# Kernel optimization log

Hardware: AMD Instinct MI355X
Metric: run time of the kernel (lower is better)

Reference implementation:

```python
import jax, jax.numpy as jnp
import numpy as np

N_CIR, N_DIS, D, H = 585, 88, 128, 8
E_CC, E_DD = 20000, 3000
EPS = 1e-16


def _gcn(x, src, dst, ew, W, b, N):
    # PyG GCNConv: add self-loops (weight 1), symmetric normalization, x @ W, scatter-add, + bias
    loop = jnp.arange(N)
    s = jnp.concatenate([src, loop])
    d = jnp.concatenate([dst, loop])
    w = jnp.concatenate([ew, jnp.ones((N,), ew.dtype)])
    deg = jax.ops.segment_sum(w, d, num_segments=N)
    dinv = jnp.where(deg > 0, jax.lax.rsqrt(deg), 0.0)
    norm = dinv[s] * w * dinv[d]                      # [E+N]
    h = x @ W                                         # [N,D]
    out = jax.ops.segment_sum(h[s] * norm[:, None], d, num_segments=N)
    return out + b


def _gat(x, src, dst, ea, W, a_src, a_dst, a_edge, We, b, N):
    # PyG GATConv(heads=H, concat=False, edge_dim=1): self-loops with mean edge_attr fill,
    # leaky_relu attention logits, segment softmax over destination, mean over heads, + bias
    loop = jnp.arange(N)
    s = jnp.concatenate([src, loop])
    d = jnp.concatenate([dst, loop])
    ea = jnp.concatenate([ea, jnp.broadcast_to(ea.mean(0, keepdims=True), (N, ea.shape[1]))], 0)
    h = (x @ W).reshape(N, H, D)                      # [N,H,D]
    e = (ea @ We).reshape(-1, H, D)                   # [E+N,H,D]
    alpha = (h * a_src).sum(-1)[s] + (h * a_dst).sum(-1)[d] + (e * a_edge).sum(-1)
    alpha = jax.nn.leaky_relu(alpha, 0.2)             # [E+N,H]
    amax = jax.ops.segment_max(alpha, d, num_segments=N)
    ex = jnp.exp(alpha - amax[d])
    den = jax.ops.segment_sum(ex, d, num_segments=N)
    alpha = ex / (den[d] + EPS)
    out = jax.ops.segment_sum(h[s] * alpha[:, :, None], d, num_segments=N)  # [N,H,D]
    return out.mean(1) + b


def _branch(x, edges, mat, gw1, gb1, aw, asrc, adst, aedge, awe, ab, gw2, gb2, N):
    src, dst = edges[0], edges[1]
    ew = mat[src, dst]                                # gather edge weights from dense matrix
    f1 = jax.nn.relu(_gcn(x, src, dst, ew, gw1, gb1, N))
    att = jax.nn.relu(_gat(f1, src, dst, ew[:, None], aw, asrc, adst, aedge, awe, ab, N))
    f2 = jax.nn.relu(_gcn(att, src, dst, ew, gw2, gb2, N))
    return f1, f2


def _cnn(f1, f2, Wk, b):
    # Conv2d(2,256,(128,1)) over [1,2,128,N] == per-node GEMM over (2,128) then view/transpose
    Xv = jnp.stack([f1.T, f2.T])                      # [2,D,N]
    return jnp.einsum('ock,ckn->no', Wk[..., 0], Xv) + b  # [N,256]


def setup_inputs():
    ks = jax.random.split(jax.random.key(0), 24)
    rn = lambda i, sh, s=1.0: jax.random.normal(ks[i], sh, jnp.float32) * s
    w = 0.08  # ~glorot scale for fan-in 128
    return {
        'x_cir': rn(0, (N_CIR, D)),
        'x_dis': rn(1, (N_DIS, D)),
        'cc_matrix': jax.random.uniform(ks[2], (N_CIR, N_CIR), jnp.float32),
        'dd_matrix': jax.random.uniform(ks[3], (N_DIS, N_DIS), jnp.float32),
        'gcn_c1_w': rn(4, (D, D), w), 'gcn_c1_b': jnp.zeros((D,), jnp.float32),
        'gat_c_w': rn(5, (D, H * D), w), 'gat_c_asrc': rn(6, (H, D), w),
        'gat_c_adst': rn(7, (H, D), w), 'gat_c_aedge': rn(8, (H, D), w),
        'gat_c_we': rn(9, (1, H * D), w), 'gat_c_b': jnp.zeros((D,), jnp.float32),
        'gcn_c2_w': rn(10, (D, D), w), 'gcn_c2_b': jnp.zeros((D,), jnp.float32),
        'gcn_d1_w': rn(11, (D, D), w), 'gcn_d1_b': jnp.zeros((D,), jnp.float32),
        'gat_d_w': rn(12, (D, H * D), w), 'gat_d_asrc': rn(13, (H, D), w),
        'gat_d_adst': rn(14, (H, D), w), 'gat_d_aedge': rn(15, (H, D), w),
        'gat_d_we': rn(16, (1, H * D), w), 'gat_d_b': jnp.zeros((D,), jnp.float32),
        'gcn_d2_w': rn(17, (D, D), w), 'gcn_d2_b': jnp.zeros((D,), jnp.float32),
        'conv_c_w': rn(18, (256, 2, D, 1), w), 'conv_c_b': jnp.zeros((256,), jnp.float32),
        'conv_d_w': rn(19, (256, 2, D, 1), w), 'conv_d_b': jnp.zeros((256,), jnp.float32),
        'cc_edges': jax.random.randint(ks[20], (2, E_CC), 0, N_CIR),
        'dd_edges': jax.random.randint(ks[21], (2, E_DD), 0, N_DIS),
    }


def reference(x_cir, x_dis, cc_matrix, dd_matrix,
              gcn_c1_w, gcn_c1_b, gat_c_w, gat_c_asrc, gat_c_adst, gat_c_aedge, gat_c_we, gat_c_b,
              gcn_c2_w, gcn_c2_b,
              gcn_d1_w, gcn_d1_b, gat_d_w, gat_d_asrc, gat_d_adst, gat_d_aedge, gat_d_we, gat_d_b,
              gcn_d2_w, gcn_d2_b,
              conv_c_w, conv_c_b, conv_d_w, conv_d_b,
              cc_edges, dd_edges):
    c1, c2 = _branch(x_cir, cc_edges, cc_matrix, gcn_c1_w, gcn_c1_b, gat_c_w, gat_c_asrc,
                     gat_c_adst, gat_c_aedge, gat_c_we, gat_c_b, gcn_c2_w, gcn_c2_b, N_CIR)
    d1, d2 = _branch(x_dis, dd_edges, dd_matrix, gcn_d1_w, gcn_d1_b, gat_d_w, gat_d_asrc,
                     gat_d_adst, gat_d_aedge, gat_d_we, gat_d_b, gcn_d2_w, gcn_d2_b, N_DIS)
    cir_fea = _cnn(c1, c2, conv_c_w, conv_c_b)        # [585,256]
    dis_fea = _cnn(d1, d2, conv_d_w, conv_d_b)        # [88,256]
    return cir_fea @ dis_fea.T, cir_fea, dis_fea
```

## Files before the change

### kernel.cpp

```cpp
#include <hip/hip_runtime.h>

constexpr int NCIR = 585;
constexpr int NDIS = 88;
constexpr int NT   = NCIR + NDIS;
constexpr int DIM  = 128;
constexpr int NH   = 8;
constexpr int ECC  = 20000;
constexpr int EDD  = 3000;
constexpr int ET   = ECC + EDD;
constexpr int CO   = 256;
constexpr int CAP  = 256;
constexpr int F1C  = (NCIR + 3) / 4;
constexpr int F1D  = (NDIS + 3) / 4;
constexpr int NG   = F1C + F1D;
constexpr int GBK  = (ET + 255) / 256;
constexpr int GEMB = (NT + 1) / 2;

__device__ __forceinline__ int decode_cnt(unsigned raw){
  return (int)(raw >= 0xA0000000u ? raw - 0xAAAAAAAAu : raw);
}

struct P {
  const float *x_c, *x_d, *mat_c, *mat_d;
  const float *g1w_c, *g1b_c, *aw_c, *as_c, *ad_c, *ae_c, *we_c, *ab_c, *g2w_c, *g2b_c;
  const float *g1w_d, *g1b_d, *aw_d, *as_d, *ad_d, *ae_d, *we_d, *ab_d, *g2w_d, *g2b_d;
  const float *cw_c, *cb_c, *cw_d, *cb_d;
  const int *csrc, *cdst, *dsrc, *ddst;
  float *hs, *hd, *h, *f1, *hg, *fill_w, *psc, *psd, *wdeg;
  unsigned *cnt;
  int *fill_s;
  float *out_score, *out_cir, *out_dis;
};

__global__ __launch_bounds__(256) void k_gg(P p){
  __shared__ float r0[256], r1[256];
  int b = blockIdx.x, t = threadIdx.x;
  if (b < GBK){
    int e = b * 256 + t;
    float wc = 0.0f, wdv = 0.0f;
    if (e < ET){
      float w; int s, d;
      if (e < ECC){
        s = p.csrc[e]; d = p.cdst[e];
        w = p.mat_c[s * NCIR + d]; wc = w;
      } else {
        int el = e - ECC;
        s = NCIR + p.dsrc[el]; d = NCIR + p.ddst[el];
        w = p.mat_d[(s - NCIR) * NDIS + (d - NCIR)]; wdv = w;
      }
      int pos = decode_cnt(atomicAdd(&p.cnt[d], 1u));
      if (pos < CAP){
        p.fill_s[d * CAP + pos] = s;
        p.fill_w[d * CAP + pos] = w;
      }
      atomicAdd(&p.wdeg[d], w);
    }
    r0[t] = wc; r1[t] = wdv;
    __syncthreads();
    for (int st = 128; st; st >>= 1){
      if (t < st){ r0[t] += r0[t + st]; r1[t] += r1[t + st]; }
      __syncthreads();
    }
    if (t == 0){ p.psc[b] = r0[0]; p.psd[b] = r1[0]; }
  } else {
    int ub = (b - GBK) * 2;
    int n = t >> 7, k = t & 127;
    int u = ub + n;
    bool ok = u < NT;
    if (ok){
      int br = u >= NCIR;
      r0[n * DIM + k] = br ? p.x_d[(u - NCIR) * DIM + k] : p.x_c[u * DIM + k];
    }
    __syncthreads();
    if (ok){
      const float* W = (u >= NCIR) ? p.g1w_d : p.g1w_c;
      float acc = 0.0f;
      #pragma unroll 8
      for (int c = 0; c < DIM; ++c) acc += r0[n * DIM + c] * W[c * DIM + k];
      p.h[u * DIM + k] = acc;
    }
  }
}

__global__ __launch_bounds__(256) void k_aggproj(P p){
  __shared__ int   deg4[4];
  __shared__ float dv4[4];
  __shared__ int   s4[4][CAP];
  __shared__ float nrm4[4][CAP];
  __shared__ float a_sh[4][DIM];
  __shared__ float wred[4][8];
  int b = blockIdx.x, t = threadIdx.x;
  int ng = b >> 2, ct = b & 3;
  int base, count, br;
  if (ng < F1C){ base = ng * 4; count = min(4, NCIR - base); br = 0; }
  else { base = NCIR + (ng - F1C) * 4; count = 4; br = 1; }
  if (t < 4){
    if (t < count){
      int u = base + t;
      deg4[t] = min(decode_cnt(p.cnt[u]), CAP);
      dv4[t]  = rsqrtf(1.0f + p.wdeg[u]);
    } else deg4[t] = 0;
  }
  __syncthreads();
  for (int idx = t; idx < 4 * CAP; idx += 256){
    int nn = idx >> 8, j = idx & (CAP - 1);
    if (j < deg4[nn]){
      int u = base + nn;
      int s = p.fill_s[u * CAP + j];
      s4[nn][j] = s;
      nrm4[nn][j] = rsqrtf(1.0f + p.wdeg[s]) * p.fill_w[u * CAP + j] * dv4[nn];
    }
  }
  __syncthreads();
  const float* B1 = br ? p.g1b_d : p.g1b_c;
  int n2 = t >> 7, k = t & 127;
  for (int r = 0; r < 2; ++r){
    int nn = n2 + r * 2;
    float v = 0.0f;
    if (nn < count){
      int u = base + nn;
      float dvu = dv4[nn];
      float acc = B1[k] + p.h[u * DIM + k] * dvu * dvu;
      int deg = deg4[nn];
      #pragma unroll 4
      for (int j = 0; j < deg; ++j)
        acc += p.h[s4[nn][j] * DIM + k] * nrm4[nn][j];
      if (ct == 0) p.f1[u * DIM + k] = acc;
      v = fmaxf(acc, 0.0f);
    }
    a_sh[nn][k] = v;
  }
  __syncthreads();
  const float* W = (br ? p.aw_d : p.aw_c) + ct * 256 + t;
  float acc[4] = {0.f, 0.f, 0.f, 0.f};
  #pragma unroll 4
  for (int c = 0; c < DIM; ++c){
    float w = W[c * 1024];
    acc[0] += a_sh[0][c] * w; acc[1] += a_sh[1][c] * w;
    acc[2] += a_sh[2][c] * w; acc[3] += a_sh[3][c] * w;
  }
  int col = ct * 256 + t;
  for (int n = 0; n < count; ++n)
    p.hg[(size_t)(base + n) * 1024 + col] = acc[n];
  const float* As = br ? p.as_d : p.as_c;
  const float* Ad = br ? p.ad_d : p.ad_c;
  float av = As[col], dw = Ad[col];
  int w = t >> 6;
  #pragma unroll
  for (int n = 0; n < 4; ++n){
    float sdot = acc[n] * av, ddot = acc[n] * dw;
    #pragma unroll
    for (int off = 32; off; off >>= 1){
      sdot += __shfl_down(sdot, off, 64);
      ddot += __shfl_down(ddot, off, 64);
    }
    if ((t & 63) == 0){ wred[w][n * 2] = sdot; wred[w][n * 2 + 1] = ddot; }
  }
  __syncthreads();
  if (t < 16){
    int g = t >> 3, v = t & 7, n = v >> 1, isd = v & 1;
    if (n < count){
      float sum = wred[g * 2][v] + wred[g * 2 + 1][v];
      float* dst = isd ? p.hd : p.hs;
      dst[(base + n) * NH + ct * 2 + g] = sum;
    }
  }
}

__global__ __launch_bounds__(256) void k_att(P p){
  __shared__ float den_sh[NH], hd_sh[NH], inv_sh[NH], wself_sh[NH], wd_sh[NH];
  __shared__ float slw_sh;
  __shared__ int   s_all[CAP];
  __shared__ float w_all[CAP];
  __shared__ float alpha_all[CAP * NH];
  __shared__ float a2[2][DIM], attv[DIM], part[2][DIM];
  int d = blockIdx.x, t = threadIdx.x;
  int g = t >> 7, k = t & 127;
  int br = d >= NCIR;
  int wv = t >> 6, lane = t & 63;
  if (t < NH){ den_sh[t] = 0.0f; hd_sh[t] = p.hd[d * NH + t]; }
  if (wv == 0){
    const float* ps = br ? p.psd : p.psc;
    float v = (lane < GBK ? ps[lane] : 0.0f) + (lane + 64 < GBK ? ps[lane + 64] : 0.0f);
    #pragma unroll
    for (int off = 32; off; off >>= 1) v += __shfl_down(v, off, 64);
    if (lane == 0) slw_sh = v / (br ? (float)EDD : (float)ECC);
  }
  if (wv >= 2){
    const float* We = br ? p.we_d : p.we_c;
    const float* Ae = br ? p.ae_d : p.ae_c;
    for (int q = 0; q < 4; ++q){
      int hh = (wv - 2) * 4 + q;
      float v = We[hh * DIM + lane] * Ae[hh * DIM + lane]
              + We[hh * DIM + 64 + lane] * Ae[hh * DIM + 64 + lane];
      #pragma unroll
      for (int off = 32; off; off >>= 1) v += __shfl_down(v, off, 64);
      if (lane == 0) wd_sh[hh] = v;
    }
  }
  int deg = min(decode_cnt(p.cnt[d]), CAP);
  for (int j = t; j < deg; j += 256){
    s_all[j] = p.fill_s[d * CAP + j];
    w_all[j] = p.fill_w[d * CAP + j];
  }
  __syncthreads();
  for (int idx = t; idx < deg * NH; idx += 256){
    int j = idx >> 3, hh = idx & 7;
    int s = s_all[j];
    float a = p.hs[s * NH + hh] + hd_sh[hh] + w_all[j] * wd_sh[hh];
    a = a > 0.0f ? a : 0.2f * a;
    float ex = expf(a);
    alpha_all[idx] = ex;
    atomicAdd(&den_sh[hh], ex);
  }
  __syncthreads();
  if (t < NH){
    float a = p.hs[d * NH + t] + hd_sh[t] + slw_sh * wd_sh[t];
    a = a > 0.0f ? a : 0.2f * a;
    float ex = expf(a);
    float inv = 1.0f / (den_sh[t] + ex + 1e-16f) * 0.125f;
    inv_sh[t] = inv;
    wself_sh[t] = ex * inv;
  }
  __syncthreads();
  for (int idx = t; idx < deg * NH; idx += 256)
    alpha_all[idx] *= inv_sh[idx & 7];
  __syncthreads();
  float acc = 0.0f;
  if (g == 0){
    acc = (br ? p.ab_d : p.ab_c)[k];
    const float* r = p.hg + (size_t)d * 1024;
    #pragma unroll
    for (int hh = 0; hh < NH; ++hh) acc += wself_sh[hh] * r[hh * DIM + k];
  }
  for (int jj = g; jj < deg; jj += 2){
    const float* r = p.hg + (size_t)s_all[jj] * 1024;
    const float* al = alpha_all + jj * NH;
    #pragma unroll
    for (int hh = 0; hh < NH; ++hh) acc += al[hh] * r[hh * DIM + k];
  }
  a2[g][k] = acc;
  __syncthreads();
  if (g == 0) attv[k] = fmaxf(a2[0][k] + a2[1][k], 0.0f);
  __syncthreads();
  const float* W = br ? p.g2w_d : p.g2w_c;
  float h2 = 0.0f;
  #pragma unroll 8
  for (int c = g * 64; c < g * 64 + 64; ++c) h2 += attv[c] * W[c * DIM + k];
  part[g][k] = h2;
  __syncthreads();
  if (g == 0) p.h[d * DIM + k] = part[0][k] + part[1][k];
}

__global__ __launch_bounds__(256) void k_fuse2(P p){
  __shared__ float s12[4][2 * DIM];
  __shared__ int   deg4[4];
  __shared__ float dv4[4];
  __shared__ int   s4[4][CAP];
  __shared__ float nrm4[4][CAP];
  int b = blockIdx.x, o = threadIdx.x;
  int gbase, count, br; float* out;
  if (b < F1C){ gbase = b * 4; count = min(4, NCIR - gbase); br = 0;
                out = p.out_cir + (size_t)gbase * CO; }
  else { int lb = (b - F1C) * 4; gbase = NCIR + lb; count = 4; br = 1;
         out = p.out_dis + (size_t)lb * CO; }
  if (o < 4){
    if (o < count){
      int u = gbase + o;
      deg4[o] = min(decode_cnt(p.cnt[u]), CAP);
      dv4[o]  = rsqrtf(1.0f + p.wdeg[u]);
    } else deg4[o] = 0;
  }
  __syncthreads();
  for (int idx = o; idx < 4 * CAP; idx += 256){
    int nn = idx >> 8, j = idx & (CAP - 1);
    if (j < deg4[nn]){
      int u = gbase + nn;
      int s = p.fill_s[u * CAP + j];
      s4[nn][j] = s;
      nrm4[nn][j] = rsqrtf(1.0f + p.wdeg[s]) * p.fill_w[u * CAP + j] * dv4[nn];
    }
  }
  __syncthreads();
  const float* B2 = br ? p.g2b_d : p.g2b_c;
  int n2 = o >> 7, k = o & 127;
  for (int r = 0; r < 2; ++r){
    int nn = n2 + r * 2;
    float v1 = 0.0f, v2 = 0.0f;
    if (nn < count){
      int u = gbase + nn;
      float dvu = dv4[nn];
      float acc = B2[k] + p.h[u * DIM + k] * dvu * dvu;
      int deg = deg4[nn];
      #pragma unroll 4
      for (int j = 0; j < deg; ++j)
        acc += p.h[s4[nn][j] * DIM + k] * nrm4[nn][j];
      v2 = fmaxf(acc, 0.0f);
      v1 = fmaxf(p.f1[u * DIM + k], 0.0f);
    }
    s12[nn][k] = v1;
    s12[nn][DIM + k] = v2;
  }
  __syncthreads();
  const float* W = (br ? p.cw_d : p.cw_c) + o * 2 * DIM;
  float bv = (br ? p.cb_d : p.cb_c)[o];
  float a0 = bv, a1 = bv, a2 = bv, a3 = bv;
  #pragma unroll 4
  for (int q = 0; q < 2 * DIM; ++q){
    float wv = W[q];
    a0 += s12[0][q] * wv; a1 += s12[1][q] * wv;
    a2 += s12[2][q] * wv; a3 += s12[3][q] * wv;
  }
  if (0 < count) out[0 * CO + o] = a0;
  if (1 < count) out[1 * CO + o] = a1;
  if (2 < count) out[2 * CO + o] = a2;
  if (3 < count) out[3 * CO + o] = a3;
}

__global__ void k_final(P p){
  __shared__ float ci[CO];
  int i = blockIdx.x, j = threadIdx.x;
  ci[j]       = p.out_cir[i * CO + j];
  ci[DIM + j] = p.out_cir[i * CO + DIM + j];
  __syncthreads();
  if (j < NDIS){
    const float* dr = p.out_dis + j * CO;
    float acc = 0.0f;
    #pragma unroll 8
    for (int q = 0; q < CO; ++q) acc += ci[q] * dr[q];
    p.out_score[i * NDIS + j] = acc;
  }
}

extern "C" void kernel_launch(void* const* d_in, const int* in_sizes, int n_in,
                              void* d_out, int out_size, void* d_ws, size_t ws_size,
                              hipStream_t stream){
  P p;
  typedef const float* F;
  p.x_c   = (F)d_in[0];  p.x_d   = (F)d_in[1];
  p.mat_c = (F)d_in[2];  p.mat_d = (F)d_in[3];
  p.g1w_c = (F)d_in[4];  p.g1b_c = (F)d_in[5];
  p.aw_c  = (F)d_in[6];  p.as_c  = (F)d_in[7];  p.ad_c = (F)d_in[8];
  p.ae_c  = (F)d_in[9];  p.we_c  = (F)d_in[10]; p.ab_c = (F)d_in[11];
  p.g2w_c = (F)d_in[12]; p.g2b_c = (F)d_in[13];
  p.g1w_d = (F)d_in[14]; p.g1b_d = (F)d_in[15];
  p.aw_d  = (F)d_in[16]; p.as_d  = (F)d_in[17]; p.ad_d = (F)d_in[18];
  p.ae_d  = (F)d_in[19]; p.we_d  = (F)d_in[20]; p.ab_d = (F)d_in[21];
  p.g2w_d = (F)d_in[22]; p.g2b_d = (F)d_in[23];
  p.cw_c  = (F)d_in[24]; p.cb_c  = (F)d_in[25];
  p.cw_d  = (F)d_in[26]; p.cb_d  = (F)d_in[27];
  const int* cc_edges = (const int*)d_in[28];
  const int* dd_edges = (const int*)d_in[29];
  p.csrc = cc_edges;  p.cdst = cc_edges + ECC;
  p.dsrc = dd_edges;  p.ddst = dd_edges + EDD;

  float* out = (float*)d_out;
  p.out_score = out;
  p.out_cir   = out + NCIR * NDIS;
  p.out_dis   = p.out_cir + NCIR * CO;

  float* w = (float*)d_ws;
  auto alloc = [&](size_t n){ float* q = w; w += n; return q; };
  p.wdeg   = alloc(676);
  p.cnt    = (unsigned*)alloc(676);
  p.psc    = alloc(92);
  p.psd    = alloc(92);
  p.hs     = alloc((size_t)NT * NH);
  p.hd     = alloc((size_t)NT * NH);
  p.h      = alloc((size_t)NT * DIM);
  p.f1     = alloc((size_t)NT * DIM);
  p.hg     = alloc((size_t)NT * 1024);
  p.fill_w = alloc((size_t)NT * CAP);
  p.fill_s = (int*)alloc((size_t)NT * CAP);

  k_gg     <<<GBK + GEMB, 256, 0, stream>>>(p);
  k_aggproj<<<NG * 4,     256, 0, stream>>>(p);
  k_att    <<<NT,         256, 0, stream>>>(p);
  k_fuse2  <<<F1C + F1D,  256, 0, stream>>>(p);
  k_final  <<<NCIR,       DIM, 0, stream>>>(p);
}
```

Baseline: 192.4 us.

## Merge five kernels into one cooperative persistent kernel with grid syncs

Replaces the five separate kernel launches with a single cooperative kernel (676 blocks) that separates the stages with grid-wide barriers, reusing one shared-memory buffer across stages. The per-branch edge-weight/attention dot products are hoisted into two dedicated blocks in the first stage instead of being recomputed in every attention block. The final score GEMM is split across 256 threads with two halves reduced in shared memory. This removes launch gaps and tail drain between kernels, but adds grid-sync cost and requires all blocks to be co-resident.

```diff
diff --git a/kernel.cpp b/kernel.cpp
--- a/kernel.cpp
+++ b/kernel.cpp
@@ -1,4 +1,7 @@
 #include <hip/hip_runtime.h>
+#include <hip/hip_cooperative_groups.h>
+
+namespace cg = cooperative_groups;
 
 constexpr int NCIR = 585;
 constexpr int NDIS = 88;
@@ -15,6 +18,7 @@
 constexpr int NG   = F1C + F1D;
 constexpr int GBK  = (ET + 255) / 256;
 constexpr int GEMB = (NT + 1) / 2;
+constexpr int GRID = NG * 4;
 
 __device__ __forceinline__ int decode_cnt(unsigned raw){
   return (int)(raw >= 0xA0000000u ? raw - 0xAAAAAAAAu : raw);
@@ -26,16 +30,20 @@
   const float *g1w_d, *g1b_d, *aw_d, *as_d, *ad_d, *ae_d, *we_d, *ab_d, *g2w_d, *g2b_d;
   const float *cw_c, *cb_c, *cw_d, *cb_d;
   const int *csrc, *cdst, *dsrc, *ddst;
-  float *hs, *hd, *h, *f1, *hg, *fill_w, *psc, *psd, *wdeg;
+  float *hs, *hd, *h, *f1, *hg, *fill_w, *psc, *psd, *wdeg, *wdall;
   unsigned *cnt;
   int *fill_s;
   float *out_score, *out_cir, *out_dis;
 };
 
-__global__ __launch_bounds__(256) void k_gg(P p){
-  __shared__ float r0[256], r1[256];
-  int b = blockIdx.x, t = threadIdx.x;
+__global__ __launch_bounds__(256, 4) void k_all(P p){
+  __shared__ __align__(16) float smem[3456];
+  cg::grid_group grid = cg::this_grid();
+  const int b = blockIdx.x, t = threadIdx.x;
+
   if (b < GBK){
+    float* r0 = smem;
+    float* r1 = smem + 256;
     int e = b * 256 + t;
     float wc = 0.0f, wdv = 0.0f;
     if (e < ET){
@@ -62,7 +70,8 @@
       __syncthreads();
     }
     if (t == 0){ p.psc[b] = r0[0]; p.psd[b] = r1[0]; }
-  } else {
+  } else if (b < GBK + GEMB){
+    float* r0 = smem;
     int ub = (b - GBK) * 2;
     int n = t >> 7, k = t & 127;
     int u = ub + n;
@@ -79,256 +88,271 @@
       for (int c = 0; c < DIM; ++c) acc += r0[n * DIM + c] * W[c * DIM + k];
       p.h[u * DIM + k] = acc;
     }
+  } else if (b < GBK + GEMB + 2){
+    int brn = b - (GBK + GEMB);
+    const float* We = brn ? p.we_d : p.we_c;
+    const float* Ae = brn ? p.ae_d : p.ae_c;
+    int hh = t >> 5, l = t & 31;
+    float v = 0.0f;
+    #pragma unroll
+    for (int q = l; q < DIM; q += 32) v += We[hh * DIM + q] * Ae[hh * DIM + q];
+    #pragma unroll
+    for (int off = 16; off; off >>= 1) v += __shfl_down(v, off, 32);
+    if (l == 0) p.wdall[brn * NH + hh] = v;
   }
-}
-
-__global__ __launch_bounds__(256) void k_aggproj(P p){
-  __shared__ int   deg4[4];
-  __shared__ float dv4[4];
-  __shared__ int   s4[4][CAP];
-  __shared__ float nrm4[4][CAP];
-  __shared__ float a_sh[4][DIM];
-  __shared__ float wred[4][8];
-  int b = blockIdx.x, t = threadIdx.x;
-  int ng = b >> 2, ct = b & 3;
-  int base, count, br;
-  if (ng < F1C){ base = ng * 4; count = min(4, NCIR - base); br = 0; }
-  else { base = NCIR + (ng - F1C) * 4; count = 4; br = 1; }
-  if (t < 4){
-    if (t < count){
-      int u = base + t;
-      deg4[t] = min(decode_cnt(p.cnt[u]), CAP);
-      dv4[t]  = rsqrtf(1.0f + p.wdeg[u]);
-    } else deg4[t] = 0;
+  grid.sync();
+
+  {
+    int*   deg4 = (int*)smem;
+    float* dv4  = smem + 4;
+    int*   s4   = (int*)(smem + 8);
+    float* nrm4 = smem + 1032;
+    float* a_sh = smem + 2056;
+    float* wred = smem + 2568;
+    int ng = b >> 2, ct = b & 3;
+    int base, count, br;
+    if (ng < F1C){ base = ng * 4; count = min(4, NCIR - base); br = 0; }
+    else { base = NCIR + (ng - F1C) * 4; count = 4; br = 1; }
+    if (t < 4){
+      if (t < count){
+        int u = base + t;
+        deg4[t] = min(decode_cnt(p.cnt[u]), CAP);
+        dv4[t]  = rsqrtf(1.0f + p.wdeg[u]);
+      } else deg4[t] = 0;
+    }
+    __syncthreads();
+    for (int idx = t; idx < 4 * CAP; idx += 256){
+      int nn = idx >> 8, j = idx & (CAP - 1);
+      if (j < deg4[nn]){
+        int u = base + nn;
+        int s = p.fill_s[u * CAP + j];
+        s4[nn * CAP + j] = s;
+        nrm4[nn * CAP + j] = rsqrtf(1.0f + p.wdeg[s]) * p.fill_w[u * CAP + j] * dv4[nn];
+      }
+    }
+    __syncthreads();
+    const float* B1 = br ? p.g1b_d : p.g1b_c;
+    int n2 = t >> 7, k = t & 127;
+    for (int r = 0; r < 2; ++r){
+      int nn = n2 + r * 2;
+      float v = 0.0f;
+      if (nn < count){
+        int u = base + nn;
+        float dvu = dv4[nn];
+        float acc = B1[k] + p.h[u * DIM + k] * dvu * dvu;
+        int deg = deg4[nn];
+        #pragma unroll 4
+        for (int j = 0; j < deg; ++j)
+          acc += p.h[s4[nn * CAP + j] * DIM + k] * nrm4[nn * CAP + j];
+        if (ct == 0) p.f1[u * DIM + k] = acc;
+        v = fmaxf(acc, 0.0f);
+      }
+      a_sh[nn * DIM + k] = v;
+    }
+    __syncthreads();
+    const float* W = (br ? p.aw_d : p.aw_c) + ct * 256 + t;
+    float acc[4] = {0.f, 0.f, 0.f, 0.f};
+    #pragma unroll 4
+    for (int c = 0; c < DIM; ++c){
+      float w = W[c * 1024];
+      acc[0] += a_sh[c] * w;           acc[1] += a_sh[DIM + c] * w;
+      acc[2] += a_sh[2 * DIM + c] * w; acc[3] += a_sh[3 * DIM + c] * w;
+    }
+    int col = ct * 256 + t;
+    for (int n = 0; n < count; ++n)
+      p.hg[(size_t)(base + n) * 1024 + col] = acc[n];
+    const float* As = br ? p.as_d : p.as_c;
+    const float* Ad = br ? p.ad_d : p.ad_c;
+    float av = As[col], dw = Ad[col];
+    int w = t >> 6;
+    #pragma unroll
+    for (int n = 0; n < 4; ++n){
+      float sdot = acc[n] * av, ddot = acc[n] * dw;
+      #pragma unroll
+      for (int off = 32; off; off >>= 1){
+        sdot += __shfl_down(sdot, off, 64);
+        ddot += __shfl_down(ddot, off, 64);
+      }
+      if ((t & 63) == 0){ wred[w * 8 + n * 2] = sdot; wred[w * 8 + n * 2 + 1] = ddot; }
+    }
+    __syncthreads();
+    if (t < 16){
+      int gq = t >> 3, v = t & 7, n = v >> 1, isd = v & 1;
+      if (n < count){
+        float sum = wred[(gq * 2) * 8 + v] + wred[(gq * 2 + 1) * 8 + v];
+        float* dst = isd ? p.hd : p.hs;
+        dst[(base + n) * NH + ct * 2 + gq] = sum;
+      }
+    }
   }
-  __syncthreads();
-  for (int idx = t; idx < 4 * CAP; idx += 256){
-    int nn = idx >> 8, j = idx & (CAP - 1);
-    if (j < deg4[nn]){
-      int u = base + nn;
-      int s = p.fill_s[u * CAP + j];
-      s4[nn][j] = s;
-      nrm4[nn][j] = rsqrtf(1.0f + p.wdeg[s]) * p.fill_w[u * CAP + j] * dv4[nn];
-    }
-  }
-  __syncthreads();
-  const float* B1 = br ? p.g1b_d : p.g1b_c;
-  int n2 = t >> 7, k = t & 127;
-  for (int r = 0; r < 2; ++r){
-    int nn = n2 + r * 2;
-    float v = 0.0f;
-    if (nn < count){
-      int u = base + nn;
-      float dvu = dv4[nn];
-      float acc = B1[k] + p.h[u * DIM + k] * dvu * dvu;
-      int deg = deg4[nn];
-      #pragma unroll 4
-      for (int j = 0; j < deg; ++j)
-        acc += p.h[s4[nn][j] * DIM + k] * nrm4[nn][j];
-      if (ct == 0) p.f1[u * DIM + k] = acc;
-      v = fmaxf(acc, 0.0f);
-    }
-    a_sh[nn][k] = v;
-  }
-  __syncthreads();
-  const float* W = (br ? p.aw_d : p.aw_c) + ct * 256 + t;
-  float acc[4] = {0.f, 0.f, 0.f, 0.f};
-  #pragma unroll 4
-  for (int c = 0; c < DIM; ++c){
-    float w = W[c * 1024];
-    acc[0] += a_sh[0][c] * w; acc[1] += a_sh[1][c] * w;
-    acc[2] += a_sh[2][c] * w; acc[3] += a_sh[3][c] * w;
-  }
-  int col = ct * 256 + t;
-  for (int n = 0; n < count; ++n)
-    p.hg[(size_t)(base + n) * 1024 + col] = acc[n];
-  const float* As = br ? p.as_d : p.as_c;
-  const float* Ad = br ? p.ad_d : p.ad_c;
-  float av = As[col], dw = Ad[col];
-  int w = t >> 6;
-  #pragma unroll
-  for (int n = 0; n < 4; ++n){
-    float sdot = acc[n] * av, ddot = acc[n] * dw;
-    #pragma unroll
-    for (int off = 32; off; off >>= 1){
-      sdot += __shfl_down(sdot, off, 64);
-      ddot += __shfl_down(ddot, off, 64);
-    }
-    if ((t & 63) == 0){ wred[w][n * 2] = sdot; wred[w][n * 2 + 1] = ddot; }
-  }
-  __syncthreads();
-  if (t < 16){
-    int g = t >> 3, v = t & 7, n = v >> 1, isd = v & 1;
-    if (n < count){
-      float sum = wred[g * 2][v] + wred[g * 2 + 1][v];
-      float* dst = isd ? p.hd : p.hs;
-      dst[(base + n) * NH + ct * 2 + g] = sum;
-    }
-  }
-}
-
-__global__ __launch_bounds__(256) void k_att(P p){
-  __shared__ float den_sh[NH], hd_sh[NH], inv_sh[NH], wself_sh[NH], wd_sh[NH];
-  __shared__ float slw_sh;
-  __shared__ int   s_all[CAP];
-  __shared__ float w_all[CAP];
-  __shared__ float alpha_all[CAP * NH];
-  __shared__ float a2[2][DIM], attv[DIM], part[2][DIM];
-  int d = blockIdx.x, t = threadIdx.x;
-  int g = t >> 7, k = t & 127;
-  int br = d >= NCIR;
-  int wv = t >> 6, lane = t & 63;
-  if (t < NH){ den_sh[t] = 0.0f; hd_sh[t] = p.hd[d * NH + t]; }
-  if (wv == 0){
-    const float* ps = br ? p.psd : p.psc;
-    float v = (lane < GBK ? ps[lane] : 0.0f) + (lane + 64 < GBK ? ps[lane + 64] : 0.0f);
-    #pragma unroll
-    for (int off = 32; off; off >>= 1) v += __shfl_down(v, off, 64);
-    if (lane == 0) slw_sh = v / (br ? (float)EDD : (float)ECC);
-  }
-  if (wv >= 2){
-    const float* We = br ? p.we_d : p.we_c;
-    const float* Ae = br ? p.ae_d : p.ae_c;
-    for (int q = 0; q < 4; ++q){
-      int hh = (wv - 2) * 4 + q;
-      float v = We[hh * DIM + lane] * Ae[hh * DIM + lane]
-              + We[hh * DIM + 64 + lane] * Ae[hh * DIM + 64 + lane];
+  grid.sync();
+
+  if (b < NT){
+    float* den_sh   = smem;
+    float* hd_sh    = smem + 8;
+    float* inv_sh   = smem + 16;
+    float* wself_sh = smem + 24;
+    float* wd_sh    = smem + 32;
+    float* slw_sh   = smem + 40;
+    int*   s_all    = (int*)(smem + 48);
+    float* w_all    = smem + 304;
+    float* alpha_all= smem + 560;
+    float* a2       = smem + 2608;
+    float* attv     = smem + 2864;
+    float* part     = smem + 2992;
+    int d = b;
+    int g = t >> 7, k = t & 127;
+    int br = d >= NCIR;
+    int wv = t >> 6, lane = t & 63;
+    if (t < NH){
+      den_sh[t] = 0.0f;
+      hd_sh[t]  = p.hd[d * NH + t];
+      wd_sh[t]  = p.wdall[br * NH + t];
+    }
+    if (wv == 0){
+      const float* ps = br ? p.psd : p.psc;
+      float v = (lane < GBK ? ps[lane] : 0.0f) + (lane + 64 < GBK ? ps[lane + 64] : 0.0f);
       #pragma unroll
       for (int off = 32; off; off >>= 1) v += __shfl_down(v, off, 64);
-      if (lane == 0) wd_sh[hh] = v;
-    }
+      if (lane == 0) slw_sh[0] = v / (br ? (float)EDD : (float)ECC);
+    }
+    int deg = min(decode_cnt(p.cnt[d]), CAP);
+    for (int j = t; j < deg; j += 256){
+      s_all[j] = p.fill_s[d * CAP + j];
+      w_all[j] = p.fill_w[d * CAP + j];
+    }
+    __syncthreads();
+    for (int idx = t; idx < deg * NH; idx += 256){
+      int j = idx >> 3, hh = idx & 7;
+      int s = s_all[j];
+      float a = p.hs[s * NH + hh] + hd_sh[hh] + w_all[j] * wd_sh[hh];
+      a = a > 0.0f ? a : 0.2f * a;
+      float ex = expf(a);
+      alpha_all[idx] = ex;
+      atomicAdd(&den_sh[hh], ex);
+    }
+    __syncthreads();
+    if (t < NH){
+      float a = p.hs[d * NH + t] + hd_sh[t] + slw_sh[0] * wd_sh[t];
+      a = a > 0.0f ? a : 0.2f * a;
+      float ex = expf(a);
+      float inv = 1.0f / (den_sh[t] + ex + 1e-16f) * 0.125f;
+      inv_sh[t] = inv;
+      wself_sh[t] = ex * inv;
+    }
+    __syncthreads();
+    for (int idx = t; idx < deg * NH; idx += 256)
+      alpha_all[idx] *= inv_sh[idx & 7];
+    __syncthreads();
+    float acc = 0.0f;
+    if (g == 0){
+      acc = (br ? p.ab_d : p.ab_c)[k];
+      const float* r = p.hg + (size_t)d * 1024;
+      #pragma unroll
+      for (int hh = 0; hh < NH; ++hh) acc += wself_sh[hh] * r[hh * DIM + k];
+    }
+    for (int jj = g; jj < deg; jj += 2){
+      const float* r = p.hg + (size_t)s_all[jj] * 1024;
+      const float* al = alpha_all + jj * NH;
+      #pragma unroll
+      for (int hh = 0; hh < NH; ++hh) acc += al[hh] * r[hh * DIM + k];
+    }
+    a2[g * DIM + k] = acc;
+    __syncthreads();
+    if (g == 0) attv[k] = fmaxf(a2[k] + a2[DIM + k], 0.0f);
+    __syncthreads();
+    const float* W = br ? p.g2w_d : p.g2w_c;
+    float h2 = 0.0f;
+    #pragma unroll 8
+    for (int c = g * 64; c < g * 64 + 64; ++c) h2 += attv[c] * W[c * DIM + k];
+    part[g * DIM + k] = h2;
+    __syncthreads();
+    if (g == 0) p.h[d * DIM + k] = part[k] + part[DIM + k];
   }
-  int deg = min(decode_cnt(p.cnt[d]), CAP);
-  for (int j = t; j < deg; j += 256){
-    s_all[j] = p.fill_s[d * CAP + j];
-    w_all[j] = p.fill_w[d * CAP + j];
+  grid.sync();
+
+  if (b < F1C + F1D){
+    float* s12  = smem;
+    int*   deg4 = (int*)(smem + 1024);
+    float* dv4  = smem + 1028;
+    int*   s4   = (int*)(smem + 1032);
+    float* nrm4 = smem + 2056;
+    int o = t;
+    int gbase, count, br; float* out;
+    if (b < F1C){ gbase = b * 4; count = min(4, NCIR - gbase); br = 0;
+                  out = p.out_cir + (size_t)gbase * CO; }
+    else { int lb = (b - F1C) * 4; gbase = NCIR + lb; count = 4; br = 1;
+           out = p.out_dis + (size_t)lb * CO; }
+    if (o < 4){
+      if (o < count){
+        int u = gbase + o;
+        deg4[o] = min(decode_cnt(p.cnt[u]), CAP);
+        dv4[o]  = rsqrtf(1.0f + p.wdeg[u]);
+      } else deg4[o] = 0;
+    }
+    __syncthreads();
+    for (int idx = o; idx < 4 * CAP; idx += 256){
+      int nn = idx >> 8, j = idx & (CAP - 1);
+      if (j < deg4[nn]){
+        int u = gbase + nn;
+        int s = p.fill_s[u * CAP + j];
+        s4[nn * CAP + j] = s;
+        nrm4[nn * CAP + j] = rsqrtf(1.0f + p.wdeg[s]) * p.fill_w[u * CAP + j] * dv4[nn];
+      }
+    }
+    __syncthreads();
+    const float* B2 = br ? p.g2b_d : p.g2b_c;
+    int n2 = o >> 7, k = o & 127;
+    for (int r = 0; r < 2; ++r){
+      int nn = n2 + r * 2;
+      float v1 = 0.0f, v2 = 0.0f;
+      if (nn < count){
+        int u = gbase + nn;
+        float dvu = dv4[nn];
+        float acc = B2[k] + p.h[u * DIM + k] * dvu * dvu;
+        int deg = deg4[nn];
+        #pragma unroll 4
+        for (int j = 0; j < deg; ++j)
+          acc += p.h[s4[nn * CAP + j] * DIM + k] * nrm4[nn * CAP + j];
+        v2 = fmaxf(acc, 0.0f);
+        v1 = fmaxf(p.f1[u * DIM + k], 0.0f);
+      }
+      s12[nn * 2 * DIM + k] = v1;
+      s12[nn * 2 * DIM + DIM + k] = v2;
+    }
+    __syncthreads();
+    const float* W = (br ? p.cw_d : p.cw_c) + o * 2 * DIM;
+    float bv = (br ? p.cb_d : p.cb_c)[o];
+    float a0 = bv, a1 = bv, a2v = bv, a3 = bv;
+    #pragma unroll 4
+    for (int q = 0; q < 2 * DIM; ++q){
+      float wv = W[q];
+      a0 += s12[q] * wv;           a1 += s12[2 * DIM + q] * wv;
+      a2v += s12[4 * DIM + q] * wv; a3 += s12[6 * DIM + q] * wv;
+    }
+    if (0 < count) out[0 * CO + o] = a0;
+    if (1 < count) out[1 * CO + o] = a1;
+    if (2 < count) out[2 * CO + o] = a2v;
+    if (3 < count) out[3 * CO + o] = a3;
   }
-  __syncthreads();
-  for (int idx = t; idx < deg * NH; idx += 256){
-    int j = idx >> 3, hh = idx & 7;
-    int s = s_all[j];
-    float a = p.hs[s * NH + hh] + hd_sh[hh] + w_all[j] * wd_sh[hh];
-    a = a > 0.0f ? a : 0.2f * a;
-    float ex = expf(a);
-    alpha_all[idx] = ex;
-    atomicAdd(&den_sh[hh], ex);
-  }
-  __syncthreads();
-  if (t < NH){
-    float a = p.hs[d * NH + t] + hd_sh[t] + slw_sh * wd_sh[t];
-    a = a > 0.0f ? a : 0.2f * a;
-    float ex = expf(a);
-    float inv = 1.0f / (den_sh[t] + ex + 1e-16f) * 0.125f;
-    inv_sh[t] = inv;
-    wself_sh[t] = ex * inv;
-  }
-  __syncthreads();
-  for (int idx = t; idx < deg * NH; idx += 256)
-    alpha_all[idx] *= inv_sh[idx & 7];
-  __syncthreads();
-  float acc = 0.0f;
-  if (g == 0){
-    acc = (br ? p.ab_d : p.ab_c)[k];
-    const float* r = p.hg + (size_t)d * 1024;
-    #pragma unroll
-    for (int hh = 0; hh < NH; ++hh) acc += wself_sh[hh] * r[hh * DIM + k];
-  }
-  for (int jj = g; jj < deg; jj += 2){
-    const float* r = p.hg + (size_t)s_all[jj] * 1024;
-    const float* al = alpha_all + jj * NH;
-    #pragma unroll
-    for (int hh = 0; hh < NH; ++hh) acc += al[hh] * r[hh * DIM + k];
-  }
-  a2[g][k] = acc;
-  __syncthreads();
-  if (g == 0) attv[k] = fmaxf(a2[0][k] + a2[1][k], 0.0f);
-  __syncthreads();
-  const float* W = br ? p.g2w_d : p.g2w_c;
-  float h2 = 0.0f;
-  #pragma unroll 8
-  for (int c = g * 64; c < g * 64 + 64; ++c) h2 += attv[c] * W[c * DIM + k];
-  part[g][k] = h2;
-  __syncthreads();
-  if (g == 0) p.h[d * DIM + k] = part[0][k] + part[1][k];
-}
-
-__global__ __launch_bounds__(256) void k_fuse2(P p){
-  __shared__ float s12[4][2 * DIM];
-  __shared__ int   deg4[4];
-  __shared__ float dv4[4];
-  __shared__ int   s4[4][CAP];
-  __shared__ float nrm4[4][CAP];
-  int b = blockIdx.x, o = threadIdx.x;
-  int gbase, count, br; float* out;
-  if (b < F1C){ gbase = b * 4; count = min(4, NCIR - gbase); br = 0;
-                out = p.out_cir + (size_t)gbase * CO; }
-  else { int lb = (b - F1C) * 4; gbase = NCIR + lb; count = 4; br = 1;
-         out = p.out_dis + (size_t)lb * CO; }
-  if (o < 4){
-    if (o < count){
-      int u = gbase + o;
-      deg4[o] = min(decode_cnt(p.cnt[u]), CAP);
-      dv4[o]  = rsqrtf(1.0f + p.wdeg[u]);
-    } else deg4[o] = 0;
-  }
-  __syncthreads();
-  for (int idx = o; idx < 4 * CAP; idx += 256){
-    int nn = idx >> 8, j = idx & (CAP - 1);
-    if (j < deg4[nn]){
-      int u = gbase + nn;
-      int s = p.fill_s[u * CAP + j];
-      s4[nn][j] = s;
-      nrm4[nn][j] = rsqrtf(1.0f + p.wdeg[s]) * p.fill_w[u * CAP + j] * dv4[nn];
-    }
-  }
-  __syncthreads();
-  const float* B2 = br ? p.g2b_d : p.g2b_c;
-  int n2 = o >> 7, k = o & 127;
-  for (int r = 0; r < 2; ++r){
-    int nn = n2 + r * 2;
-    float v1 = 0.0f, v2 = 0.0f;
-    if (nn < count){
-      int u = gbase + nn;
-      float dvu = dv4[nn];
-      float acc = B2[k] + p.h[u * DIM + k] * dvu * dvu;
-      int deg = deg4[nn];
-      #pragma unroll 4
-      for (int j = 0; j < deg; ++j)
-        acc += p.h[s4[nn][j] * DIM + k] * nrm4[nn][j];
-      v2 = fmaxf(acc, 0.0f);
-      v1 = fmaxf(p.f1[u * DIM + k], 0.0f);
-    }
-    s12[nn][k] = v1;
-    s12[nn][DIM + k] = v2;
-  }
-  __syncthreads();
-  const float* W = (br ? p.cw_d : p.cw_c) + o * 2 * DIM;
-  float bv = (br ? p.cb_d : p.cb_c)[o];
-  float a0 = bv, a1 = bv, a2 = bv, a3 = bv;
-  #pragma unroll 4
-  for (int q = 0; q < 2 * DIM; ++q){
-    float wv = W[q];
-    a0 += s12[0][q] * wv; a1 += s12[1][q] * wv;
-    a2 += s12[2][q] * wv; a3 += s12[3][q] * wv;
-  }
-  if (0 < count) out[0 * CO + o] = a0;
-  if (1 < count) out[1 * CO + o] = a1;
-  if (2 < count) out[2 * CO + o] = a2;
-  if (3 < count) out[3 * CO + o] = a3;
-}
-
-__global__ void k_final(P p){
-  __shared__ float ci[CO];
-  int i = blockIdx.x, j = threadIdx.x;
-  ci[j]       = p.out_cir[i * CO + j];
-  ci[DIM + j] = p.out_cir[i * CO + DIM + j];
-  __syncthreads();
-  if (j < NDIS){
-    const float* dr = p.out_dis + j * CO;
-    float acc = 0.0f;
-    #pragma unroll 8
-    for (int q = 0; q < CO; ++q) acc += ci[q] * dr[q];
-    p.out_score[i * NDIS + j] = acc;
+  grid.sync();
+
+  if (b < NCIR){
+    float* ci  = smem;
+    float* fin = smem + 256;
+    ci[t] = p.out_cir[b * CO + t];
+    __syncthreads();
+    int half = t >> 7, j = t & 127;
+    if (j < NDIS){
+      const float* dr = p.out_dis + j * CO + half * DIM;
+      const float* cc = ci + half * DIM;
+      float acc = 0.0f;
+      #pragma unroll 8
+      for (int q = 0; q < DIM; ++q) acc += cc[q] * dr[q];
+      fin[half * NDIS + j] = acc;
+    }
+    __syncthreads();
+    if (t < NDIS) p.out_score[b * NDIS + t] = fin[t] + fin[NDIS + t];
   }
 }
 
@@ -365,6 +389,7 @@
   p.cnt    = (unsigned*)alloc(676);
   p.psc    = alloc(92);
   p.psd    = alloc(92);
+  p.wdall  = alloc(16);
   p.hs     = alloc((size_t)NT * NH);
   p.hd     = alloc((size_t)NT * NH);
   p.h      = alloc((size_t)NT * DIM);
@@ -373,9 +398,6 @@
   p.fill_w = alloc((size_t)NT * CAP);
   p.fill_s = (int*)alloc((size_t)NT * CAP);
 
-  k_gg     <<<GBK + GEMB, 256, 0, stream>>>(p);
-  k_aggproj<<<NG * 4,     256, 0, stream>>>(p);
-  k_att    <<<NT,         256, 0, stream>>>(p);
-  k_fuse2  <<<F1C + F1D,  256, 0, stream>>>(p);
-  k_final  <<<NCIR,       DIM, 0, stream>>>(p);
+  void* args[] = { (void*)&p };
+  hipLaunchCooperativeKernel((const void*)k_all, dim3(GRID), dim3(256), args, 0, stream);
 }
```

Measured after the change: 538.5 us. +179.9%, slower.
